# Optimization experiments

Hardware: AMD Instinct MI355X
Metric: run time of the kernel (lower is better)

The kernel has to match this reference:

```python
import jax, jax.numpy as jnp
import numpy as np

N, F_IN, T, E, O = 50000, 32, 8, 800000, 32


def setup_inputs() -> dict:
    ks = jax.random.split(jax.random.key(0), 16)
    s = 0.05
    return {
        "X": jax.random.normal(ks[0], (N, F_IN, T), dtype=jnp.float32),
        "edge_index": jax.random.randint(ks[1], (2, E), 0, N, dtype=jnp.int64),
        "edge_weight": jax.random.uniform(ks[2], (E,), dtype=jnp.float32),
        # GCNConv weights for z/r/h gates: lin weight [O, F_IN], bias [O]
        "Wz": jax.random.normal(ks[3], (O, F_IN), dtype=jnp.float32) * s,
        "bz": jnp.zeros((O,), dtype=jnp.float32),
        "Wr": jax.random.normal(ks[4], (O, F_IN), dtype=jnp.float32) * s,
        "br": jnp.zeros((O,), dtype=jnp.float32),
        "Wh": jax.random.normal(ks[5], (O, F_IN), dtype=jnp.float32) * s,
        "bh": jnp.zeros((O,), dtype=jnp.float32),
        # Linear(2*O, O) per gate
        "Lz": jax.random.normal(ks[6], (O, 2 * O), dtype=jnp.float32) * s,
        "lz_b": jnp.zeros((O,), dtype=jnp.float32),
        "Lr": jax.random.normal(ks[7], (O, 2 * O), dtype=jnp.float32) * s,
        "lr_b": jnp.ones((O,), dtype=jnp.float32),
        "Lh": jax.random.normal(ks[8], (O, 2 * O), dtype=jnp.float32) * s,
        "lh_b": jnp.zeros((O,), dtype=jnp.float32),
        "attention": jax.random.uniform(ks[9], (T,), dtype=jnp.float32),
    }


def reference(X, edge_index, edge_weight, Wz, bz, Wr, br, Wh, bh,
              Lz, lz_b, Lr, lr_b, Lh, lh_b, attention):
    n = X.shape[0]
    # --- GCN normalization with self-loops (computed once; graph is static) ---
    loop = jnp.arange(n, dtype=edge_index.dtype)
    row = jnp.concatenate([edge_index[0], loop])
    col = jnp.concatenate([edge_index[1], loop])
    ew = jnp.concatenate([edge_weight, jnp.ones((n,), dtype=X.dtype)])
    deg = jax.ops.segment_sum(ew, col, num_segments=n)
    deg_safe = jnp.where(deg > 0, deg, 1.0)
    dinv = jnp.where(deg > 0, jax.lax.rsqrt(deg_safe), 0.0)
    norm = dinv[row] * ew * dinv[col]  # [E+N]

    def conv(x, W, b):
        h = x @ W.T                                   # [N, O]
        msg = norm[:, None] * h[row]                  # gather over sources
        return jax.ops.segment_sum(msg, col, num_segments=n) + b

    def tgcn_cell(x, H):
        Z = jax.nn.sigmoid(jnp.concatenate([conv(x, Wz, bz), H], axis=1) @ Lz.T + lz_b)
        R = jax.nn.sigmoid(jnp.concatenate([conv(x, Wr, br), H], axis=1) @ Lr.T + lr_b)
        H_tilde = jnp.tanh(jnp.concatenate([conv(x, Wh, bh), H * R], axis=1) @ Lh.T + lh_b)
        return Z * H + (1.0 - Z) * H_tilde

    H0 = jnp.zeros((n, Lz.shape[0]), dtype=X.dtype)   # hidden init (H=None)
    probs = jax.nn.softmax(attention)
    Xs = jnp.moveaxis(X, 2, 0)                        # [T, N, F]

    def step(acc, inp):
        x_t, p = inp
        return acc + p * tgcn_cell(x_t, H0), None

    H_accum, _ = jax.lax.scan(step, H0, (Xs, probs))
    return H_accum
```

## Files before the change

### kernel.cpp

```cpp
#include <hip/hip_runtime.h>
#include <hip/hip_fp16.h>
#include <math.h>


#define GATH16(EV, WT)                                                     \
  {                                                                        \
    unsigned voff = ((unsigned)(EV) << 9) | loff;                          \
    uint2 q = *(const uint2*)((const char*)Xh + voff);                     \
    __half2 ha = *(__half2*)&q.x;                                          \
    __half2 hb = *(__half2*)&q.y;                                          \
    acc.x = fmaf((WT), __low2float(ha),  acc.x);                           \
    acc.y = fmaf((WT), __high2float(ha), acc.y);                           \
    acc.z = fmaf((WT), __low2float(hb),  acc.z);                           \
    acc.w = fmaf((WT), __high2float(hb), acc.w);                           \
  }

#define GATHV(V)                                                           \
  {                                                                        \
    int   src_ = (int)(unsigned)(V);                                       \
    float wt_  = __uint_as_float((unsigned)((V) >> 32));                   \
    GATH16(src_, wt_);                                                     \
  }

__device__ inline void do_prep(int g, int tid,
    const float* __restrict__ Wz, const float* __restrict__ bz,
    const float* __restrict__ Wh, const float* __restrict__ bh,
    const float* __restrict__ Lz, const float* __restrict__ lzb,
    const float* __restrict__ Lh, const float* __restrict__ lhb,
    const float* __restrict__ att,
    float* __restrict__ Mt, float* __restrict__ cvec, float* __restrict__ p) {
  const float* L  = g ? Lh  : Lz;
  const float* W  = g ? Wh  : Wz;
  const float* bb = g ? bh  : bz;
  const float* lb = g ? lhb : lzb;
  int o = tid & 31;
  for (int f = tid >> 5; f < 32; f += 8) {
    float s = 0.f;
    for (int k = 0; k < 32; ++k) s += L[o * 64 + k] * W[k * 32 + f];
    Mt[g * 1024 + f * 32 + o] = s;
  }
  if (tid < 32) {
    float c = lb[tid];
    for (int k = 0; k < 32; ++k) c += L[tid * 64 + k] * bb[k];
    cvec[g * 32 + tid] = c;
  }
  if (g == 0 && tid == 0) {
    float m = att[0];
    for (int t = 1; t < 8; ++t) m = fmaxf(m, att[t]);
    float e8[8], sm = 0.f;
    for (int t = 0; t < 8; ++t) { e8[t] = expf(att[t] - m); sm += e8[t]; }
    for (int t = 0; t < 8; ++t) p[t] = e8[t] / sm;
  }
}

__global__ __launch_bounds__(256) void k1_slot(
    const int* __restrict__ ei, const float* __restrict__ ew,
    unsigned long long* __restrict__ pk, int2* __restrict__ slot, int cap,
    const float* __restrict__ Wz, const float* __restrict__ bz,
    const float* __restrict__ Wh, const float* __restrict__ bh,
    const float* __restrict__ Lz, const float* __restrict__ lzb,
    const float* __restrict__ Lh, const float* __restrict__ lhb,
    const float* __restrict__ att,
    float* __restrict__ Mt, float* __restrict__ cvec, float* __restrict__ p,
    int E) {
  int b = blockIdx.x;
  int tid = threadIdx.x;
  if (b < 2) { do_prep(b, tid, Wz, bz, Wh, bh, Lz, lzb, Lh, lhb, att, Mt, cvec, p); return; }
  int e = (b - 2) * 256 + tid;
  if (e < E) {
    int r = ei[e];
    int c = ei[E + e];
    float w = ew[e];
    unsigned wfx = (unsigned)(w * 16777216.0f + 0.5f);
    unsigned long long old =
        atomicAdd(pk + c, ((unsigned long long)wfx << 32) | 1ull);
    unsigned pos = (unsigned)(old & 0xffffffffull);
    if (pos < (unsigned)cap) {
      unsigned long long v =
          ((unsigned long long)__float_as_uint(w) << 32) | (unsigned)r;
      __builtin_nontemporal_store(
          v, (unsigned long long*)(slot + (size_t)c * cap + pos));
    }
  }
}

__global__ __launch_bounds__(256) void k2_conv(
    const float* __restrict__ X, const unsigned long long* __restrict__ pk,
    __half* __restrict__ Xh, long n8) {
  long i = blockIdx.x * (long)blockDim.x + threadIdx.x;
  if (i < n8) {
    int node = (int)(i >> 5);
    unsigned long long v = pk[node];
    float di = rsqrtf((float)(v >> 32) * (1.0f / 16777216.0f) + 1.0f);
    const float4* Xv = (const float4*)X;
    float4 a = Xv[2 * i], c = Xv[2 * i + 1];
    union { int4 i4; __half2 h[4]; } u;
    u.h[0] = __floats2half2_rn(di * a.x, di * a.y);
    u.h[1] = __floats2half2_rn(di * a.z, di * a.w);
    u.h[2] = __floats2half2_rn(di * c.x, di * c.y);
    u.h[3] = __floats2half2_rn(di * c.z, di * c.w);
    ((int4*)Xh)[i] = u.i4;
  }
}

__global__ __launch_bounds__(64) void k3_main(
    const __half* __restrict__ Xh, const unsigned long long* __restrict__ pk,
    const int2* __restrict__ slot, int cap,
    const float* __restrict__ Mt, const float* __restrict__ cvec,
    const float* __restrict__ p, float* __restrict__ out) {
  int node = blockIdx.x;
  int l = threadIdx.x;
  __shared__ float ax[256];

  unsigned long long v = pk[node];
  int cnt = (int)(v & 0xffffffffull);
  if (cnt > cap) cnt = cap;
  float di = rsqrtf((float)(v >> 32) * (1.0f / 16777216.0f) + 1.0f);

  float4 acc = make_float4(0.f, 0.f, 0.f, 0.f);
  unsigned loff = (unsigned)l << 3;

  GATH16(node, 1.0f);
  const unsigned long long* row =
      (const unsigned long long*)(slot + (size_t)node * cap);
  int j = 0;
  for (; j + 7 < cnt; j += 8) {
    unsigned long long v0 = __builtin_nontemporal_load(row + j);
    unsigned long long v1 = __builtin_nontemporal_load(row + j + 1);
    unsigned long long v2 = __builtin_nontemporal_load(row + j + 2);
    unsigned long long v3 = __builtin_nontemporal_load(row + j + 3);
    unsigned long long v4 = __builtin_nontemporal_load(row + j + 4);
    unsigned long long v5 = __builtin_nontemporal_load(row + j + 5);
    unsigned long long v6 = __builtin_nontemporal_load(row + j + 6);
    unsigned long long v7 = __builtin_nontemporal_load(row + j + 7);
    GATHV(v0);
    GATHV(v1);
    GATHV(v2);
    GATHV(v3);
    GATHV(v4);
    GATHV(v5);
    GATHV(v6);
    GATHV(v7);
  }
  for (; j < cnt; ++j) {
    unsigned long long v0 = __builtin_nontemporal_load(row + j);
    GATHV(v0);
  }
  acc.x *= di; acc.y *= di; acc.z *= di; acc.w *= di;

  ((float4*)ax)[l] = acc;
  __syncthreads();

  int o = l & 31, g = l >> 5;
  float c = cvec[g * 32 + o];
  float pre[8];
#pragma unroll
  for (int t = 0; t < 8; ++t) pre[t] = c;

  const float*  M   = Mt + g * 1024;
  const float4* axv = (const float4*)ax;
#pragma unroll 8
  for (int f = 0; f < 32; ++f) {
    float  m  = M[f * 32 + o];
    float4 a0 = axv[f * 2];
    float4 a1 = axv[f * 2 + 1];
    pre[0] = fmaf(m, a0.x, pre[0]); pre[1] = fmaf(m, a0.y, pre[1]);
    pre[2] = fmaf(m, a0.z, pre[2]); pre[3] = fmaf(m, a0.w, pre[3]);
    pre[4] = fmaf(m, a1.x, pre[4]); pre[5] = fmaf(m, a1.y, pre[5]);
    pre[6] = fmaf(m, a1.z, pre[6]); pre[7] = fmaf(m, a1.w, pre[7]);
  }

  float vv[8];
  if (g == 0) {
#pragma unroll
    for (int t = 0; t < 8; ++t)
      vv[t] = __builtin_amdgcn_rcpf(1.f + __expf(pre[t]));
  } else {
#pragma unroll
    for (int t = 0; t < 8; ++t)
      vv[t] = 1.f - 2.f * __builtin_amdgcn_rcpf(__expf(2.f * pre[t]) + 1.f);
  }

  float res = 0.f;
#pragma unroll
  for (int t = 0; t < 8; ++t) {
    float other = __shfl(vv[t], l ^ 32);
    res += p[t] * vv[t] * other;
  }
  if (g == 0)
    __builtin_nontemporal_store(res, out + (size_t)node * 32 + o);
}


extern "C" void kernel_launch(void* const* d_in, const int* in_sizes, int n_in,
                              void* d_out, int out_size, void* d_ws, size_t ws_size,
                              hipStream_t stream) {
  const float* X   = (const float*)d_in[0];
  const int*   ei  = (const int*)d_in[1];
  const float* ew  = (const float*)d_in[2];
  const float* Wz  = (const float*)d_in[3];
  const float* bz  = (const float*)d_in[4];
  const float* Wh  = (const float*)d_in[7];
  const float* bh  = (const float*)d_in[8];
  const float* Lz  = (const float*)d_in[9];
  const float* lzb = (const float*)d_in[10];
  const float* Lh  = (const float*)d_in[13];
  const float* lhb = (const float*)d_in[14];
  const float* att = (const float*)d_in[15];

  int N = in_sizes[0] / 256;
  int E = in_sizes[2];
  (void)n_in; (void)out_size;

  long n8  = (long)N * 32;
  int  nbe = (E + 255) / 256;
  int  nbc = (int)((n8 + 255) / 256);

  size_t off = 0;
  auto al = [&](size_t b) { size_t q = off; off = (off + b + 255) & ~(size_t)255; return q; };
  size_t o_pk  = al((size_t)N * 8);
  size_t o_mt  = al(2048 * 4);
  size_t o_cv  = al(64 * 4);
  size_t o_p   = al(8 * 4);
  size_t o_xh  = al((size_t)N * 256 * 2);
  size_t fixed = off;
  int cap = 0;
  for (int c : {64, 48, 32}) {
    if (fixed + (size_t)N * c * 8 <= ws_size) { cap = c; break; }
  }
  if (!cap) return;

  char* w = (char*)d_ws;
  unsigned long long* pk = (unsigned long long*)(w + o_pk);
  float* Mt   = (float*)(w + o_mt);
  float* cvec = (float*)(w + o_cv);
  float* p    = (float*)(w + o_p);
  __half* Xh  = (__half*)(w + o_xh);
  int2*  slot = (int2*)(w + fixed);

  (void)hipMemsetAsync(pk, 0, (size_t)N * 8, stream);
  k1_slot<<<2 + nbe, 256, 0, stream>>>(ei, ew, pk, slot, cap,
                                       Wz, bz, Wh, bh, Lz, lzb, Lh, lhb,
                                       att, Mt, cvec, p, E);
  k2_conv<<<nbc, 256, 0, stream>>>(X, pk, Xh, n8);
  k3_main<<<N, 64, 0, stream>>>(Xh, pk, slot, cap, Mt, cvec, p,
                                (float*)d_out);
}
```

Before: 141.8 us.

## Fold source degree scaling into edge weights and fuse fp16 conversion with slot build

The fp16 conversion of X no longer depends on degrees, so it is merged into the edge-slot kernel as extra blocks, and edge blocks now process four edges per thread. A new per-node kernel rescales each stored edge weight by the source node's inverse square-root degree. The main kernel then applies the self-loop degree factor directly, and the nontemporal loads and stores are replaced with plain ones. This removes one dependent kernel stage but adds another launch over all nodes that rereads and rewrites the slot array.

```diff
diff --git a/kernel.cpp b/kernel.cpp
--- a/kernel.cpp
+++ b/kernel.cpp
@@ -13,13 +13,6 @@
     acc.y = fmaf((WT), __high2float(ha), acc.y);                           \
     acc.z = fmaf((WT), __low2float(hb),  acc.z);                           \
     acc.w = fmaf((WT), __high2float(hb), acc.w);                           \
-  }
-
-#define GATHV(V)                                                           \
-  {                                                                        \
-    int   src_ = (int)(unsigned)(V);                                       \
-    float wt_  = __uint_as_float((unsigned)((V) >> 32));                   \
-    GATH16(src_, wt_);                                                     \
   }
 
 __device__ inline void do_prep(int g, int tid,
@@ -53,53 +46,69 @@
   }
 }
 
-__global__ __launch_bounds__(256) void k1_slot(
-    const int* __restrict__ ei, const float* __restrict__ ew,
-    unsigned long long* __restrict__ pk, int2* __restrict__ slot, int cap,
+__global__ __launch_bounds__(256) void kA(
+    const float* __restrict__ X, const int* __restrict__ ei,
+    const float* __restrict__ ew, unsigned long long* __restrict__ pk,
+    int2* __restrict__ slot, int cap, __half* __restrict__ Xh,
     const float* __restrict__ Wz, const float* __restrict__ bz,
     const float* __restrict__ Wh, const float* __restrict__ bh,
     const float* __restrict__ Lz, const float* __restrict__ lzb,
     const float* __restrict__ Lh, const float* __restrict__ lhb,
     const float* __restrict__ att,
     float* __restrict__ Mt, float* __restrict__ cvec, float* __restrict__ p,
-    int E) {
+    int E, long n8, int nbe4) {
   int b = blockIdx.x;
   int tid = threadIdx.x;
   if (b < 2) { do_prep(b, tid, Wz, bz, Wh, bh, Lz, lzb, Lh, lhb, att, Mt, cvec, p); return; }
-  int e = (b - 2) * 256 + tid;
-  if (e < E) {
-    int r = ei[e];
-    int c = ei[E + e];
-    float w = ew[e];
-    unsigned wfx = (unsigned)(w * 16777216.0f + 0.5f);
-    unsigned long long old =
-        atomicAdd(pk + c, ((unsigned long long)wfx << 32) | 1ull);
-    unsigned pos = (unsigned)(old & 0xffffffffull);
-    if (pos < (unsigned)cap) {
-      unsigned long long v =
-          ((unsigned long long)__float_as_uint(w) << 32) | (unsigned)r;
-      __builtin_nontemporal_store(
-          v, (unsigned long long*)(slot + (size_t)c * cap + pos));
+  b -= 2;
+  if (b < nbe4) {
+    int base = b * 1024 + tid;
+#pragma unroll
+    for (int k = 0; k < 4; ++k) {
+      int e = base + k * 256;
+      if (e < E) {
+        int r = ei[e];
+        int c = ei[E + e];
+        float w = ew[e];
+        unsigned wfx = (unsigned)(w * 16777216.0f + 0.5f);
+        unsigned long long old =
+            atomicAdd(pk + c, ((unsigned long long)wfx << 32) | 1ull);
+        unsigned pos = (unsigned)(old & 0xffffffffull);
+        if (pos < (unsigned)cap)
+          slot[(size_t)c * cap + pos] = make_int2(r, __float_as_int(w));
+      }
     }
-  }
-}
-
-__global__ __launch_bounds__(256) void k2_conv(
-    const float* __restrict__ X, const unsigned long long* __restrict__ pk,
-    __half* __restrict__ Xh, long n8) {
-  long i = blockIdx.x * (long)blockDim.x + threadIdx.x;
+    return;
+  }
+  b -= nbe4;
+  long i = (long)b * 256 + tid;
   if (i < n8) {
-    int node = (int)(i >> 5);
-    unsigned long long v = pk[node];
-    float di = rsqrtf((float)(v >> 32) * (1.0f / 16777216.0f) + 1.0f);
     const float4* Xv = (const float4*)X;
     float4 a = Xv[2 * i], c = Xv[2 * i + 1];
     union { int4 i4; __half2 h[4]; } u;
-    u.h[0] = __floats2half2_rn(di * a.x, di * a.y);
-    u.h[1] = __floats2half2_rn(di * a.z, di * a.w);
-    u.h[2] = __floats2half2_rn(di * c.x, di * c.y);
-    u.h[3] = __floats2half2_rn(di * c.z, di * c.w);
+    u.h[0] = __floats2half2_rn(a.x, a.y);
+    u.h[1] = __floats2half2_rn(a.z, a.w);
+    u.h[2] = __floats2half2_rn(c.x, c.y);
+    u.h[3] = __floats2half2_rn(c.z, c.w);
     ((int4*)Xh)[i] = u.i4;
+  }
+}
+
+__global__ __launch_bounds__(64) void kD(
+    const unsigned long long* __restrict__ pk, int2* __restrict__ slot,
+    int cap) {
+  int node = blockIdx.x;
+  int l = threadIdx.x;
+  unsigned long long v = pk[node];
+  int cnt = (int)(v & 0xffffffffull);
+  if (cnt > cap) cnt = cap;
+  if (l < cnt) {
+    size_t idx = (size_t)node * cap + l;
+    int2 s = slot[idx];
+    unsigned long long pv = pk[s.x];
+    float dis = rsqrtf((float)(pv >> 32) * (1.0f / 16777216.0f) + 1.0f);
+    s.y = __float_as_int(__int_as_float(s.y) * dis);
+    slot[idx] = s;
   }
 }
 
@@ -120,31 +129,24 @@
   float4 acc = make_float4(0.f, 0.f, 0.f, 0.f);
   unsigned loff = (unsigned)l << 3;
 
-  GATH16(node, 1.0f);
-  const unsigned long long* row =
-      (const unsigned long long*)(slot + (size_t)node * cap);
+  GATH16(node, di);
+  const int2* row = slot + (size_t)node * cap;
   int j = 0;
   for (; j + 7 < cnt; j += 8) {
-    unsigned long long v0 = __builtin_nontemporal_load(row + j);
-    unsigned long long v1 = __builtin_nontemporal_load(row + j + 1);
-    unsigned long long v2 = __builtin_nontemporal_load(row + j + 2);
-    unsigned long long v3 = __builtin_nontemporal_load(row + j + 3);
-    unsigned long long v4 = __builtin_nontemporal_load(row + j + 4);
-    unsigned long long v5 = __builtin_nontemporal_load(row + j + 5);
-    unsigned long long v6 = __builtin_nontemporal_load(row + j + 6);
-    unsigned long long v7 = __builtin_nontemporal_load(row + j + 7);
-    GATHV(v0);
-    GATHV(v1);
-    GATHV(v2);
-    GATHV(v3);
-    GATHV(v4);
-    GATHV(v5);
-    GATHV(v6);
-    GATHV(v7);
+    int2 e0 = row[j],     e1 = row[j + 1], e2 = row[j + 2], e3 = row[j + 3];
+    int2 e4 = row[j + 4], e5 = row[j + 5], e6 = row[j + 6], e7 = row[j + 7];
+    GATH16(e0.x, __int_as_float(e0.y));
+    GATH16(e1.x, __int_as_float(e1.y));
+    GATH16(e2.x, __int_as_float(e2.y));
+    GATH16(e3.x, __int_as_float(e3.y));
+    GATH16(e4.x, __int_as_float(e4.y));
+    GATH16(e5.x, __int_as_float(e5.y));
+    GATH16(e6.x, __int_as_float(e6.y));
+    GATH16(e7.x, __int_as_float(e7.y));
   }
   for (; j < cnt; ++j) {
-    unsigned long long v0 = __builtin_nontemporal_load(row + j);
-    GATHV(v0);
+    int2 e0 = row[j];
+    GATH16(e0.x, __int_as_float(e0.y));
   }
   acc.x *= di; acc.y *= di; acc.z *= di; acc.w *= di;
 
@@ -187,8 +189,7 @@
     float other = __shfl(vv[t], l ^ 32);
     res += p[t] * vv[t] * other;
   }
-  if (g == 0)
-    __builtin_nontemporal_store(res, out + (size_t)node * 32 + o);
+  if (g == 0) out[(size_t)node * 32 + o] = res;
 }
 
 
@@ -212,9 +213,9 @@
   int E = in_sizes[2];
   (void)n_in; (void)out_size;
 
-  long n8  = (long)N * 32;
-  int  nbe = (E + 255) / 256;
-  int  nbc = (int)((n8 + 255) / 256);
+  long n8   = (long)N * 32;
+  int  nbe4 = (E + 1023) / 1024;
+  int  nbc  = (int)((n8 + 255) / 256);
 
   size_t off = 0;
   auto al = [&](size_t b) { size_t q = off; off = (off + b + 255) & ~(size_t)255; return q; };
@@ -239,10 +240,10 @@
   int2*  slot = (int2*)(w + fixed);
 
   (void)hipMemsetAsync(pk, 0, (size_t)N * 8, stream);
-  k1_slot<<<2 + nbe, 256, 0, stream>>>(ei, ew, pk, slot, cap,
-                                       Wz, bz, Wh, bh, Lz, lzb, Lh, lhb,
-                                       att, Mt, cvec, p, E);
-  k2_conv<<<nbc, 256, 0, stream>>>(X, pk, Xh, n8);
+  kA<<<2 + nbe4 + nbc, 256, 0, stream>>>(X, ei, ew, pk, slot, cap, Xh,
+                                         Wz, bz, Wh, bh, Lz, lzb, Lh, lhb,
+                                         att, Mt, cvec, p, E, n8, nbe4);
+  kD<<<N, 64, 0, stream>>>(pk, slot, cap);
   k3_main<<<N, 64, 0, stream>>>(Xh, pk, slot, cap, Mt, cvec, p,
                                 (float*)d_out);
 }
```

Result: no change. 139.2 us (-1.8%).
